# Optimization experiments

Hardware: AMD Instinct MI355X
Metric: run time of the kernel (lower is better)

Reference implementation:

```python
import jax, jax.numpy as jnp
import numpy as np

B, T = 32, 1024
TEMP_IN, STAT_IN = 128, 64
TEMP_OUT, STAT_OUT = 128, 64
EPS = 1e-5
NEG_SLOPE = 0.01


def _bn_eval(x, gamma, beta, mean, var):
    # BatchNorm1d in eval mode (running stats)
    return (x - mean) * jax.lax.rsqrt(var + EPS) * gamma + beta


def _leaky_relu(x):
    return jnp.where(x >= 0, x, NEG_SLOPE * x)


def setup_inputs() -> dict:
    key = jax.random.key(0)
    k = jax.random.split(key, 6)
    # deterministic ragged lengths in [512, 1024]
    lengths_np = (512 + (np.arange(B) * 37) % 513).astype(np.int64)
    N = int(lengths_np.sum())  # 23450
    batch_idx = np.repeat(np.arange(B), lengths_np).astype(np.int32)
    pos_idx = np.concatenate([np.arange(l) for l in lengths_np]).astype(np.int32)
    valid = (np.arange(T)[None, :] < lengths_np[:, None])  # [B, T]
    mask_repeat = valid[:, :, None] & valid[:, None, :]    # [B, T, T]

    inp = {
        "x_temp": jax.random.normal(k[0], (N, TEMP_IN), jnp.float32),
        "x_stat": jax.random.normal(k[1], (B, STAT_IN), jnp.float32),
        "temp_attn": jax.random.normal(k[2], (B, T, T), jnp.float32) * 0.1,
        "mask_repeat": jnp.asarray(mask_repeat),
        "lengths": jnp.asarray(lengths_np),
        "batch_idx": jnp.asarray(batch_idx),
        "pos_idx": jnp.asarray(pos_idx),
        # non_linear_temp: Linear(TEMP_IN+STAT_IN -> TEMP_OUT) + BN
        "W1": jax.random.normal(k[3], (TEMP_OUT, TEMP_IN + STAT_IN), jnp.float32) / np.sqrt(TEMP_IN + STAT_IN),
        "b1": jnp.zeros((TEMP_OUT,), jnp.float32),
        "gamma1": jnp.ones((TEMP_OUT,), jnp.float32),
        "beta1": jnp.zeros((TEMP_OUT,), jnp.float32),
        "mean1": jnp.zeros((TEMP_OUT,), jnp.float32),
        "var1": jnp.ones((TEMP_OUT,), jnp.float32),
        # non_linear_stat: Linear(STAT_IN -> STAT_OUT) + BN
        "W2": jax.random.normal(k[4], (STAT_OUT, STAT_IN), jnp.float32) / np.sqrt(STAT_IN),
        "b2": jnp.zeros((STAT_OUT,), jnp.float32),
        "gamma2": jnp.ones((STAT_OUT,), jnp.float32),
        "beta2": jnp.zeros((STAT_OUT,), jnp.float32),
        "mean2": jnp.zeros((STAT_OUT,), jnp.float32),
        "var2": jnp.ones((STAT_OUT,), jnp.float32),
    }
    return inp


def reference(x_temp, x_stat, temp_attn, mask_repeat, lengths, batch_idx, pos_idx,
              W1, b1, gamma1, beta1, mean1, var1,
              W2, b2, gamma2, beta2, mean2, var2):
    # repeat_static_features: gather per-batch static feats to packed rows
    x_stat_rep = x_stat[batch_idx]                              # [N, STAT_IN]
    h = jnp.concatenate((x_temp, x_stat_rep), axis=-1) @ W1.T + b1
    h = _leaky_relu(_bn_eval(h, gamma1, beta1, mean1, var1))    # [N, TEMP_OUT]

    # pad_packed_sequences: scatter packed rows into [B, T, C] (zeros elsewhere)
    padded = jnp.zeros((B, T, TEMP_OUT), h.dtype).at[batch_idx, pos_idx].set(h)

    # self attention: softmax(x x^T / sqrt(d)) over padded rows (as original)
    d = jnp.asarray(TEMP_OUT, h.dtype)
    qk = jnp.einsum('btc,bsc->bts', padded, padded) / jnp.sqrt(d)
    self_attn = jax.nn.softmax(qk, axis=-1)

    attn = jnp.where(mask_repeat, self_attn + temp_attn, jnp.asarray(0.0, h.dtype))

    x_stat_out = _leaky_relu(_bn_eval(x_stat @ W2.T + b2, gamma2, beta2, mean2, var2))

    x_out_pad = jnp.einsum('bts,bsc->btc', attn, padded)        # [B, T, TEMP_OUT]
    # pack_padded_sequences: gather valid positions back to packed layout
    x_out = x_out_pad[batch_idx, pos_idx]                       # [N, TEMP_OUT]
    return (x_out, x_stat_out)
```

## Files before the change

kernel.cpp:

```cpp
#include <hip/hip_runtime.h>
#include <hip/hip_bf16.h>
#include <hip/hip_fp16.h>

typedef __hip_bfloat16 bf16;
typedef __attribute__((ext_vector_type(8))) short short8;
typedef __attribute__((ext_vector_type(4))) float f32x4;

#define EPS 1e-5f
#define NSLOPE 0.01f
#define NSMAX 3

__device__ __forceinline__ float b2f(bf16 v) { return __bfloat162float(v); }
__device__ __forceinline__ float bs2f(unsigned short s) {
  bf16 t; __builtin_memcpy(&t, &s, 2); return __bfloat162float(t);
}
__device__ __forceinline__ float ld1(const void* p, size_t idx, int isbf) {
  if (isbf) return b2f(((const bf16*)p)[idx]);
  return ((const float*)p)[idx];
}
__device__ __forceinline__ void st1(void* p, size_t idx, int isbf, float v) {
  if (isbf) ((bf16*)p)[idx] = __float2bfloat16(v);
  else      ((float*)p)[idx] = v;
}
__device__ __forceinline__ short f2bs(float x) {
  bf16 t = __float2bfloat16(x);
  short s; __builtin_memcpy(&s, &t, 2); return s;
}
__device__ __forceinline__ short8 pack8f(const float* p) {
  float4 a = *(const float4*)p, b = *(const float4*)(p + 4);
  short8 r;
  r[0] = f2bs(a.x); r[1] = f2bs(a.y); r[2] = f2bs(a.z); r[3] = f2bs(a.w);
  r[4] = f2bs(b.x); r[5] = f2bs(b.y); r[6] = f2bs(b.z); r[7] = f2bs(b.w);
  return r;
}

__global__ void meta_kernel(const void* __restrict__ xt,
                            const int* __restrict__ bidx, const int* __restrict__ pidx,
                            int N, int B, int* __restrict__ rs, int* __restrict__ ln,
                            int* __restrict__ flag,
                            const void* __restrict__ W1, bf16* __restrict__ w1b, int w1n,
                            const void* __restrict__ xstat, const void* __restrict__ W2,
                            const void* __restrict__ b2, const void* __restrict__ g2,
                            const void* __restrict__ be2, const void* __restrict__ mn2,
                            const void* __restrict__ vr2, void* __restrict__ out,
                            long long obase) {
  int isbf_l = 0;
  {
    unsigned w = ((const unsigned*)xt)[threadIdx.x & 63];
    unsigned lo = w & 0xffffu;
    unsigned ex = (lo >> 7) & 0xffu;
    bool sane = ((lo & 0x7fffu) == 0u) || (ex >= 96u && ex <= 134u);
    unsigned long long m = __ballot(sane);
    isbf_l = (__popcll(m) >= 48) ? 1 : 0;
    if (blockIdx.x == 0 && threadIdx.x == 0) flag[0] = isbf_l;
  }
  int stride = gridDim.x * blockDim.x;
  int g0 = blockIdx.x * blockDim.x + threadIdx.x;
  for (int i = g0; i < N; i += stride) {
    int b = bidx[i];
    if ((unsigned)b >= (unsigned)B) continue;
    if (i == 0 || bidx[i - 1] != b) rs[b] = i;
    if (i == N - 1 || bidx[i + 1] != b) ln[b] = pidx[i] + 1;
  }
  for (int i = g0; i < w1n; i += stride) {
    int o = i / 192, k = i - o * 192;
    int ct = o >> 4, n = o & 15;
    int ks = k >> 5, rem = k & 31;
    int q = rem >> 3, j = rem & 7;
    int fi = ((ct * 6 + ks) * 64 + q * 16 + n) * 8 + j;
    w1b[fi] = __float2bfloat16(ld1(W1, i, isbf_l));
  }
  __shared__ float xs[64];
  if (threadIdx.x < 64 && blockIdx.x < B)
    xs[threadIdx.x] = ld1(xstat, blockIdx.x * 64 + threadIdx.x, isbf_l);
  __syncthreads();
  if (threadIdx.x < 64 && blockIdx.x < B) {
    const int o = threadIdx.x, bb = blockIdx.x;
    float acc = ld1(b2, o, isbf_l);
#pragma unroll 8
    for (int j = 0; j < 64; ++j) acc += xs[j] * ld1(W2, o * 64 + j, isbf_l);
    float k1 = ld1(g2, o, isbf_l) * rsqrtf(ld1(vr2, o, isbf_l) + EPS);
    float k0 = ld1(be2, o, isbf_l) - ld1(mn2, o, isbf_l) * k1;
    float v = acc * k1 + k0;
    v = (v >= 0.f) ? v : NSLOPE * v;
    st1(out, (size_t)(obase + bb * 64 + o), isbf_l, v);
  }
}

__global__ void zfill_kernel(void* out, const int* __restrict__ flag, long long n) {
  const int isbf = flag[0];
  long long i = (long long)blockIdx.x * blockDim.x + threadIdx.x;
  long long stride = (long long)gridDim.x * blockDim.x;
  for (; i < n; i += stride) st1(out, (size_t)i, isbf, 0.f);
}

__global__ __launch_bounds__(256) void h_mfma_kernel(
    const void* __restrict__ xt, const void* __restrict__ xsg,
    const int* __restrict__ bidx, const bf16* __restrict__ w1b,
    const void* __restrict__ b1,
    const void* __restrict__ g1, const void* __restrict__ be1,
    const void* __restrict__ mn1, const void* __restrict__ vr1,
    const int* __restrict__ flag, bf16* __restrict__ hout, int N) {
  const int isbf = flag[0];
  const int tid = threadIdx.x, lane = tid & 63, wv = tid >> 6;
  const int m16 = lane & 15, quad = lane >> 4;
  const int row0 = blockIdx.x * 64 + wv * 16;
  const int m = row0 + m16;
  const int mc = (m < N) ? m : (N - 1);
  const int bi = bidx[mc];

  short8 af[6];
  if (isbf) {
    const bf16* xr = (const bf16*)xt + (size_t)mc * 128 + quad * 8;
#pragma unroll
    for (int ks = 0; ks < 4; ++ks) af[ks] = *(const short8*)(xr + ks * 32);
    const bf16* sr = (const bf16*)xsg + (size_t)bi * 64 + quad * 8;
    af[4] = *(const short8*)sr;
    af[5] = *(const short8*)(sr + 32);
  } else {
    const float* xr = (const float*)xt + (size_t)mc * 128 + quad * 8;
#pragma unroll
    for (int ks = 0; ks < 4; ++ks) af[ks] = pack8f(xr + ks * 32);
    const float* sr = (const float*)xsg + (size_t)bi * 64 + quad * 8;
    af[4] = pack8f(sr);
    af[5] = pack8f(sr + 32);
  }

  f32x4 acc[8];
#pragma unroll
  for (int ct = 0; ct < 8; ++ct) acc[ct] = (f32x4){0.f, 0.f, 0.f, 0.f};

  const short8* wf = (const short8*)w1b;
#pragma unroll
  for (int ks = 0; ks < 6; ++ks) {
#pragma unroll
    for (int ct = 0; ct < 8; ++ct) {
      short8 bfrag = wf[(ct * 6 + ks) * 64 + lane];
      acc[ct] = __builtin_amdgcn_mfma_f32_16x16x32_bf16(af[ks], bfrag, acc[ct], 0, 0, 0);
    }
  }

#pragma unroll
  for (int ct = 0; ct < 8; ++ct) {
    const int o = ct * 16 + m16;
    float k1 = ld1(g1, o, isbf) * rsqrtf(ld1(vr1, o, isbf) + EPS);
    float k0 = ld1(be1, o, isbf) - ld1(mn1, o, isbf) * k1;
    float bias = ld1(b1, o, isbf);
#pragma unroll
    for (int r = 0; r < 4; ++r) {
      int mr = row0 + quad * 4 + r;
      if (mr < N) {
        float v = (acc[ct][r] + bias) * k1 + k0;
        v = (v >= 0.f) ? v : NSLOPE * v;
        hout[(size_t)mr * 128 + o] = __float2bfloat16(v);
      }
    }
  }
}

__global__ __launch_bounds__(256, 2) void attn_part_kernel(
    const void* __restrict__ ta, const bf16* __restrict__ h,
    const int* __restrict__ rs_arr, const int* __restrict__ ln_arr,
    const int* __restrict__ flag,
    unsigned short* __restrict__ accp_buf, unsigned short* __restrict__ acct_buf,
    float* __restrict__ ms_buf, float* __restrict__ ls_buf,
    int T, int N, int TT) {
  __shared__ __align__(16) unsigned short vT[128][72];
  __shared__ __align__(16) unsigned short Pw[4][16][72];

  const int b = blockIdx.y;
  const int tt = blockIdx.x / NSMAX, sl = blockIdx.x % NSMAX;
  const int t0 = tt * 64;
  const int len = ln_arr[b];
  if (t0 >= len) return;
  const int nchunk = (len + 63) >> 6;
  const int ns = (nchunk + 5) / 6;
  if (sl >= ns) return;
  const int c_begin = (sl * nchunk) / ns;
  const int c_end = ((sl + 1) * nchunk) / ns;

  const int isbf = flag[0];
  const int rs = rs_arr[b];
  const int tid = threadIdx.x;
  const int lane = tid & 63, wv = tid >> 6;
  const int m16 = lane & 15, quad = lane >> 4;
  const int t0w = t0 + wv * 16;

  short8 qf[4];
  {
    int qrow = rs + t0w + m16;
    if (qrow > N - 1) qrow = N - 1;
    const bf16* qp = h + (size_t)qrow * 128 + quad * 8;
#pragma unroll
    for (int ks = 0; ks < 4; ++ks) qf[ks] = *(const short8*)(qp + ks * 32);
  }

  const float scale = 0.08838834764831845f;
  const short8 zero8 = {0, 0, 0, 0, 0, 0, 0, 0};
  const uint4 zz = {0, 0, 0, 0};
  const size_t tarow = ((size_t)b * T + (t0w + m16)) * (size_t)T;
  const int c8base = wv * 32;

  f32x4 accp[8], acct[8];
#pragma unroll
  for (int ct = 0; ct < 8; ++ct) {
    accp[ct] = (f32x4){0.f, 0.f, 0.f, 0.f};
    acct[ct] = (f32x4){0.f, 0.f, 0.f, 0.f};
  }
  float mrun[4], lrun[4];
#pragma unroll
  for (int r = 0; r < 4; ++r) { mrun[r] = -INFINITY; lrun[r] = 0.f; }

  {
    int srow = c_begin * 64 + lane;
    bool v = srow < len;
    const bf16* src = h + (size_t)(rs + (v ? srow : 0)) * 128;
#pragma unroll
    for (int it = 0; it < 4; ++it) {
      int c8 = c8base + it * 8;
      uint4 u = v ? *(const uint4*)(src + c8) : zz;
      const unsigned short* a = (const unsigned short*)&u;
#pragma unroll
      for (int j = 0; j < 8; ++j) vT[c8 + j][lane] = a[j];
    }
  }
  __syncthreads();

  for (int ci = c_begin; ci < c_end; ++ci) {
    const int s0 = ci << 6;
    const bool have_next = (ci + 1 < c_end);

    uint4 su0 = zz, su1 = zz, su2 = zz, su3 = zz;
    if (have_next) {
      int srow = s0 + 64 + lane;
      bool v = srow < len;
      const bf16* src = h + (size_t)(rs + (v ? srow : 0)) * 128;
      if (v) {
        su0 = *(const uint4*)(src + c8base);
        su1 = *(const uint4*)(src + c8base + 8);
        su2 = *(const uint4*)(src + c8base + 16);
        su3 = *(const uint4*)(src + c8base + 24);
      }
    }

    short8 taf0, taf1;
    if (isbf) {
      const bf16* tp = (const bf16*)ta + tarow + s0 + quad * 8;
      taf0 = *(const short8*)tp;
      taf1 = *(const short8*)(tp + 32);
    } else {
      const float* tp = (const float*)ta + tarow + s0 + quad * 8;
      taf0 = pack8f(tp);
      taf1 = pack8f(tp + 32);
    }

    f32x4 sa[4];
    bool sval[4];
#pragma unroll
    for (int st = 0; st < 4; ++st) {
      int srow = s0 + st * 16 + m16;
      bool v = srow < len;
      sval[st] = v;
      const bf16* kp = h + (size_t)(rs + (v ? srow : 0)) * 128 + quad * 8;
      f32x4 a0 = (f32x4){0.f, 0.f, 0.f, 0.f};
#pragma unroll
      for (int ks = 0; ks < 4; ++ks) {
        short8 kf = v ? *(const short8*)(kp + ks * 32) : zero8;
        a0 = __builtin_amdgcn_mfma_f32_16x16x32_bf16(qf[ks], kf, a0, 0, 0, 0);
      }
      sa[st] = a0;
    }

    float cm[4];
#pragma unroll
    for (int r = 0; r < 4; ++r) cm[r] = -INFINITY;
#pragma unroll
    for (int st = 0; st < 4; ++st) {
#pragma unroll
      for (int r = 0; r < 4; ++r)
        cm[r] = fmaxf(cm[r], sval[st] ? sa[st][r] * scale : -INFINITY);
    }
#pragma unroll
    for (int off = 1; off <= 8; off <<= 1) {
#pragma unroll
      for (int r = 0; r < 4; ++r) cm[r] = fmaxf(cm[r], __shfl_xor(cm[r], off, 64));
    }
    float al[4], csum[4];
#pragma unroll
    for (int r = 0; r < 4; ++r) {
      float mnew = fmaxf(mrun[r], cm[r]);
      al[r] = __expf(mrun[r] - mnew);
      mrun[r] = mnew;
      csum[r] = 0.f;
    }
#pragma unroll
    for (int st = 0; st < 4; ++st) {
#pragma unroll
      for (int r = 0; r < 4; ++r) {
        float pv = sval[st] ? __expf(sa[st][r] * scale - mrun[r]) : 0.f;
        csum[r] += pv;
        Pw[wv][quad * 4 + r][st * 16 + m16] = (unsigned short)f2bs(pv);
      }
    }
#pragma unroll
    for (int off = 1; off <= 8; off <<= 1) {
#pragma unroll
      for (int r = 0; r < 4; ++r) csum[r] += __shfl_xor(csum[r], off, 64);
    }
#pragma unroll
    for (int r = 0; r < 4; ++r) lrun[r] = lrun[r] * al[r] + csum[r];

#pragma unroll
    for (int ct = 0; ct < 8; ++ct) {
#pragma unroll
      for (int r = 0; r < 4; ++r) accp[ct][r] *= al[r];
    }

#pragma unroll
    for (int ks = 0; ks < 2; ++ks) {
      short8 pf = *(const short8*)&Pw[wv][m16][ks * 32 + quad * 8];
      short8 tf = ks ? taf1 : taf0;
#pragma unroll
      for (int ct = 0; ct < 8; ++ct) {
        short8 bfv = *(const short8*)&vT[ct * 16 + m16][ks * 32 + quad * 8];
        accp[ct] = __builtin_amdgcn_mfma_f32_16x16x32_bf16(pf, bfv, accp[ct], 0, 0, 0);
        acct[ct] = __builtin_amdgcn_mfma_f32_16x16x32_bf16(tf, bfv, acct[ct], 0, 0, 0);
      }
    }

    if (have_next) {
      __syncthreads();
      const unsigned short* a0 = (const unsigned short*)&su0;
      const unsigned short* a1 = (const unsigned short*)&su1;
      const unsigned short* a2 = (const unsigned short*)&su2;
      const unsigned short* a3 = (const unsigned short*)&su3;
#pragma unroll
      for (int j = 0; j < 8; ++j) {
        vT[c8base + j][lane]      = a0[j];
        vT[c8base + 8 + j][lane]  = a1[j];
        vT[c8base + 16 + j][lane] = a2[j];
        vT[c8base + 24 + j][lane] = a3[j];
      }
      __syncthreads();
    }
  }

  const int slot = (b * TT + tt) * NSMAX + sl;
  const size_t abase = (size_t)slot * 8192;
#pragma unroll
  for (int r = 0; r < 4; ++r) {
    const int row = wv * 16 + quad * 4 + r;
#pragma unroll
    for (int ct = 0; ct < 8; ++ct) {
      const size_t o = abase + (size_t)row * 128 + ct * 16 + m16;
      accp_buf[o] = (unsigned short)f2bs(accp[ct][r]);
      acct_buf[o] = (unsigned short)f2bs(acct[ct][r]);
    }
    if (m16 == 0) {
      ms_buf[(size_t)slot * 64 + row] = mrun[r];
      ls_buf[(size_t)slot * 64 + row] = lrun[r];
    }
  }
}

__global__ __launch_bounds__(256) void attn_red_kernel(
    const unsigned short* __restrict__ accp_buf,
    const unsigned short* __restrict__ acct_buf,
    const float* __restrict__ ms_buf, const float* __restrict__ ls_buf,
    const int* __restrict__ rs_arr, const int* __restrict__ ln_arr,
    const int* __restrict__ flag, void* __restrict__ xout, int T, int TT) {
  const int b = blockIdx.y, tt = blockIdx.x, t0 = tt * 64;
  const int len = ln_arr[b];
  if (t0 >= len) return;
  const int isbf = flag[0];
  const int rs = rs_arr[b];
  const int nchunk = (len + 63) >> 6;
  const int ns = (nchunk + 5) / 6;
  const int base_slot = (b * TT + tt) * NSMAX;

  const int r = threadIdx.x >> 2;
  const int cg = threadIdx.x & 3;
  const int trow = t0 + r;
  if (trow >= len) return;

  float m0 = ms_buf[(size_t)(base_slot + 0) * 64 + r];
  float m1 = (ns > 1) ? ms_buf[(size_t)(base_slot + 1) * 64 + r] : -INFINITY;
  float m2 = (ns > 2) ? ms_buf[(size_t)(base_slot + 2) * 64 + r] : -INFINITY;
  float M = fmaxf(m0, fmaxf(m1, m2));
  float w0 = __expf(m0 - M);
  float w1 = (ns > 1) ? __expf(m1 - M) : 0.f;
  float w2 = (ns > 2) ? __expf(m2 - M) : 0.f;
  float L = ls_buf[(size_t)(base_slot + 0) * 64 + r] * w0;
  if (ns > 1) L += ls_buf[(size_t)(base_slot + 1) * 64 + r] * w1;
  if (ns > 2) L += ls_buf[(size_t)(base_slot + 2) * 64 + r] * w2;

  float m_f = (len < T) ? fmaxf(M, 0.f) : M;
  float corr = __expf(M - m_f);
  float l_f = L * corr + (float)(T - len) * __expf(-m_f);
  float os = corr / l_f;

  const size_t p0 = (size_t)(base_slot + 0) * 8192 + (size_t)r * 128 + cg * 32;
  const size_t p1 = (size_t)(base_slot + 1) * 8192 + (size_t)r * 128 + cg * 32;
  const size_t p2 = (size_t)(base_slot + 2) * 8192 + (size_t)r * 128 + cg * 32;
  const size_t ob = (size_t)(rs + trow) * 128 + cg * 32;

#pragma unroll
  for (int g = 0; g < 4; ++g) {
    float acc[8], tac[8];
    {
      short8 ap = *(const short8*)&accp_buf[p0 + g * 8];
      short8 at = *(const short8*)&acct_buf[p0 + g * 8];
#pragma unroll
      for (int j = 0; j < 8; ++j) {
        acc[j] = bs2f((unsigned short)ap[j]) * w0;
        tac[j] = bs2f((unsigned short)at[j]);
      }
    }
    if (ns > 1) {
      short8 ap = *(const short8*)&accp_buf[p1 + g * 8];
      short8 at = *(const short8*)&acct_buf[p1 + g * 8];
#pragma unroll
      for (int j = 0; j < 8; ++j) {
        acc[j] += bs2f((unsigned short)ap[j]) * w1;
        tac[j] += bs2f((unsigned short)at[j]);
      }
    }
    if (ns > 2) {
      short8 ap = *(const short8*)&accp_buf[p2 + g * 8];
      short8 at = *(const short8*)&acct_buf[p2 + g * 8];
#pragma unroll
      for (int j = 0; j < 8; ++j) {
        acc[j] += bs2f((unsigned short)ap[j]) * w2;
        tac[j] += bs2f((unsigned short)at[j]);
      }
    }
#pragma unroll
    for (int j = 0; j < 8; ++j)
      st1(xout, ob + g * 8 + j, isbf, acc[j] * os + tac[j]);
  }
}

__global__ __launch_bounds__(256, 2) void attn_mfma_kernel(
    const void* __restrict__ ta, const bf16* __restrict__ h,
    const int* __restrict__ rs_arr, const int* __restrict__ ln_arr,
    const int* __restrict__ flag, void* __restrict__ xout, int T, int N) {
  __shared__ __align__(16) unsigned short vT[2][128][72];
  __shared__ __align__(16) unsigned short Pw[4][16][72];

  const int b = blockIdx.y, t0 = blockIdx.x * 64;
  const int len = ln_arr[b];
  if (t0 >= len) return;
  const int isbf = flag[0];
  const int rs = rs_arr[b];
  const int tid = threadIdx.x;
  const int lane = tid & 63, wv = tid >> 6;
  const int m16 = lane & 15, quad = lane >> 4;
  const int t0w = t0 + wv * 16;

  short8 qf[4];
  {
    int qrow = rs + t0w + m16;
    if (qrow > N - 1) qrow = N - 1;
    const bf16* qp = h + (size_t)qrow * 128 + quad * 8;
#pragma unroll
    for (int ks = 0; ks < 4; ++ks) qf[ks] = *(const short8*)(qp + ks * 32);
  }

  const float scale = 0.08838834764831845f;
  const short8 zero8 = {0, 0, 0, 0, 0, 0, 0, 0};
  const uint4 zz = {0, 0, 0, 0};
  const size_t tarow = ((size_t)b * T + (t0w + m16)) * (size_t)T;
  const int c8base = wv * 32;

  f32x4 accp[8], acct[8];
#pragma unroll
  for (int ct = 0; ct < 8; ++ct) {
    accp[ct] = (f32x4){0.f, 0.f, 0.f, 0.f};
    acct[ct] = (f32x4){0.f, 0.f, 0.f, 0.f};
  }
  float mrun[4], lrun[4];
#pragma unroll
  for (int r = 0; r < 4; ++r) { mrun[r] = -INFINITY; lrun[r] = 0.f; }

  {
    int srow = lane;
    bool v = srow < len;
    const bf16* src = h + (size_t)(rs + (v ? srow : 0)) * 128;
#pragma unroll
    for (int it = 0; it < 4; ++it) {
      int c8 = c8base + it * 8;
      uint4 u = v ? *(const uint4*)(src + c8) : zz;
      const unsigned short* a = (const unsigned short*)&u;
#pragma unroll
      for (int j = 0; j < 8; ++j) vT[0][c8 + j][lane] = a[j];
    }
  }
  __syncthreads();

  const int nchunk = (len + 63) >> 6;
  for (int ci = 0; ci < nchunk; ++ci) {
    const int s0 = ci << 6;
    const int p = ci & 1;
    const bool have_next = (ci + 1 < nchunk);

    uint4 su0 = zz, su1 = zz, su2 = zz, su3 = zz;
    if (have_next) {
      int srow = s0 + 64 + lane;
      bool v = srow < len;
      const bf16* src = h + (size_t)(rs + (v ? srow : 0)) * 128;
      if (v) {
        su0 = *(const uint4*)(src + c8base);
        su1 = *(const uint4*)(src + c8base + 8);
        su2 = *(const uint4*)(src + c8base + 16);
        su3 = *(const uint4*)(src + c8base + 24);
      }
    }

    short8 taf0, taf1;
    if (isbf) {
      const bf16* tp = (const bf16*)ta + tarow + s0 + quad * 8;
      taf0 = *(const short8*)tp;
      taf1 = *(const short8*)(tp + 32);
    } else {
      const float* tp = (const float*)ta + tarow + s0 + quad * 8;
      taf0 = pack8f(tp);
      taf1 = pack8f(tp + 32);
    }

    f32x4 sa[4];
    bool sval[4];
#pragma unroll
    for (int st = 0; st < 4; ++st) {
      int srow = s0 + st * 16 + m16;
      bool v = srow < len;
      sval[st] = v;
      const bf16* kp = h + (size_t)(rs + (v ? srow : 0)) * 128 + quad * 8;
      f32x4 a0 = (f32x4){0.f, 0.f, 0.f, 0.f};
#pragma unroll
      for (int ks = 0; ks < 4; ++ks) {
        short8 kf = v ? *(const short8*)(kp + ks * 32) : zero8;
        a0 = __builtin_amdgcn_mfma_f32_16x16x32_bf16(qf[ks], kf, a0, 0, 0, 0);
      }
      sa[st] = a0;
    }

    float cm[4];
#pragma unroll
    for (int r = 0; r < 4; ++r) cm[r] = -INFINITY;
#pragma unroll
    for (int st = 0; st < 4; ++st) {
#pragma unroll
      for (int r = 0; r < 4; ++r)
        cm[r] = fmaxf(cm[r], sval[st] ? sa[st][r] * scale : -INFINITY);
    }
#pragma unroll
    for (int off = 1; off <= 8; off <<= 1) {
#pragma unroll
      for (int r = 0; r < 4; ++r) cm[r] = fmaxf(cm[r], __shfl_xor(cm[r], off, 64));
    }
    float al[4], csum[4];
#pragma unroll
    for (int r = 0; r < 4; ++r) {
      float mnew = fmaxf(mrun[r], cm[r]);
      al[r] = __expf(mrun[r] - mnew);
      mrun[r] = mnew;
      csum[r] = 0.f;
    }
#pragma unroll
    for (int st = 0; st < 4; ++st) {
#pragma unroll
      for (int r = 0; r < 4; ++r) {
        float pv = sval[st] ? __expf(sa[st][r] * scale - mrun[r]) : 0.f;
        csum[r] += pv;
        Pw[wv][quad * 4 + r][st * 16 + m16] = (unsigned short)f2bs(pv);
      }
    }
#pragma unroll
    for (int off = 1; off <= 8; off <<= 1) {
#pragma unroll
      for (int r = 0; r < 4; ++r) csum[r] += __shfl_xor(csum[r], off, 64);
    }
#pragma unroll
    for (int r = 0; r < 4; ++r) lrun[r] = lrun[r] * al[r] + csum[r];

#pragma unroll
    for (int ct = 0; ct < 8; ++ct) {
#pragma unroll
      for (int r = 0; r < 4; ++r) accp[ct][r] *= al[r];
    }

#pragma unroll
    for (int ks = 0; ks < 2; ++ks) {
      short8 pf = *(const short8*)&Pw[wv][m16][ks * 32 + quad * 8];
      short8 tf = ks ? taf1 : taf0;
#pragma unroll
      for (int ct = 0; ct < 8; ++ct) {
        short8 bfv = *(const short8*)&vT[p][ct * 16 + m16][ks * 32 + quad * 8];
        accp[ct] = __builtin_amdgcn_mfma_f32_16x16x32_bf16(pf, bfv, accp[ct], 0, 0, 0);
        acct[ct] = __builtin_amdgcn_mfma_f32_16x16x32_bf16(tf, bfv, acct[ct], 0, 0, 0);
      }
    }

    if (have_next) {
      const unsigned short* a0 = (const unsigned short*)&su0;
      const unsigned short* a1 = (const unsigned short*)&su1;
      const unsigned short* a2 = (const unsigned short*)&su2;
      const unsigned short* a3 = (const unsigned short*)&su3;
#pragma unroll
      for (int j = 0; j < 8; ++j) {
        vT[p ^ 1][c8base + j][lane]      = a0[j];
        vT[p ^ 1][c8base + 8 + j][lane]  = a1[j];
        vT[p ^ 1][c8base + 16 + j][lane] = a2[j];
        vT[p ^ 1][c8base + 24 + j][lane] = a3[j];
      }
    }
    __syncthreads();
  }

  const int nr = len - t0w;
#pragma unroll
  for (int r = 0; r < 4; ++r) {
    int t = quad * 4 + r;
    if (t < nr) {
      float m_r = mrun[r], l_r = lrun[r];
      float m_f = (len < T) ? fmaxf(m_r, 0.f) : m_r;
      float corr = __expf(m_r - m_f);
      float l_f = l_r * corr + (float)(T - len) * __expf(-m_f);
      float os = corr / l_f;
      size_t ob = (size_t)(rs + t0w + t) * 128;
#pragma unroll
      for (int ct = 0; ct < 8; ++ct)
        st1(xout, ob + ct * 16 + m16, isbf, accp[ct][r] * os + acct[ct][r]);
    }
  }
}

extern "C" void kernel_launch(void* const* d_in, const int* in_sizes, int n_in,
                              void* d_out, int out_size, void* d_ws, size_t ws_size,
                              hipStream_t stream) {
  const void* x_temp    = d_in[0];
  const void* x_stat    = d_in[1];
  const void* temp_attn = d_in[2];
  const int N = in_sizes[0] / 128;
  const int B = in_sizes[1] / 64;
  long long tt = (long long)in_sizes[2] / B;
  int T = 1; while ((long long)(T + 1) * (T + 1) <= tt) ++T;
  const int TT = (T + 63) >> 6;

  int p = 3;
  while (p < n_in && in_sizes[p] != N) ++p;
  const int* batch_idx = (const int*)d_in[p++];
  const int* pos_idx   = (const int*)d_in[p++];
  const void* W1 = d_in[p++];
  const void* b1 = d_in[p++];
  const void* g1 = d_in[p++];
  const void* be1= d_in[p++];
  const void* mn1= d_in[p++];
  const void* vr1= d_in[p++];
  const void* W2 = d_in[p++];
  const void* b2 = d_in[p++];
  const void* g2 = d_in[p++];
  const void* be2= d_in[p++];
  const void* mn2= d_in[p++];
  const void* vr2= d_in[p++];

  int*  meta = (int*)d_ws;
  int*  rs   = meta;
  int*  lnp  = meta + B;
  int*  flag = meta + 2 * B;
  size_t off = 1024;
  bf16* h    = (bf16*)((char*)d_ws + off);  off += (size_t)N * 128 * 2;
  const int w1n = 128 * 192;
  bf16* w1b  = (bf16*)((char*)d_ws + off);  off += (size_t)w1n * 2;
  off = (off + 255) & ~(size_t)255;
  size_t need_min = off;
  const size_t nslot = (size_t)B * TT * NSMAX;
  unsigned short* accp_buf = (unsigned short*)((char*)d_ws + off);
  off += nslot * 8192 * 2;
  unsigned short* acct_buf = (unsigned short*)((char*)d_ws + off);
  off += nslot * 8192 * 2;
  float* ms_buf = (float*)((char*)d_ws + off);  off += nslot * 64 * 4;
  float* ls_buf = (float*)((char*)d_ws + off);  off += nslot * 64 * 4;
  size_t need_split = off;

  long long obase = (long long)N * 128;

  meta_kernel<<<90, 256, 0, stream>>>(x_temp, batch_idx, pos_idx, N, B, rs, lnp,
                                      flag, W1, w1b, w1n,
                                      x_stat, W2, b2, g2, be2, mn2, vr2,
                                      d_out, obase);
  if (ws_size >= need_min) {
    h_mfma_kernel<<<(N + 63) / 64, 256, 0, stream>>>(x_temp, x_stat, batch_idx,
                                                     w1b, b1, g1, be1, mn1, vr1,
                                                     flag, h, N);
    if (ws_size >= need_split) {
      attn_part_kernel<<<dim3(TT * NSMAX, B), 256, 0, stream>>>(
          temp_attn, h, rs, lnp, flag, accp_buf, acct_buf, ms_buf, ls_buf,
          T, N, TT);
      attn_red_kernel<<<dim3(TT, B), 256, 0, stream>>>(
          accp_buf, acct_buf, ms_buf, ls_buf, rs, lnp, flag, d_out, T, TT);
    } else {
      attn_mfma_kernel<<<dim3(TT, B), 256, 0, stream>>>(
          temp_attn, h, rs, lnp, flag, d_out, T, N);
    }
  } else {
    zfill_kernel<<<512, 256, 0, stream>>>(d_out, flag, obase);
  }
}
```

Measured before the change: 424.9 us.

## Widen attention key chunk from 64 to 128 rows per iteration

The split-K flash attention kernel now processes 128 key rows per loop iteration instead of 64. The V-transpose tile in LDS is doubled and the P buffer is laid out as two halves. This halves the number of online-softmax rescales and block barriers per row block, and the partition count is recomputed to match in both kernels. In exchange it uses more registers (8 score tiles, 8 prefetched uint4 values, 4 temp_attn fragments) and more LDS, which may lower occupancy under launch_bounds(256,2).

```diff
diff --git a/kernel.cpp b/kernel.cpp
--- a/kernel.cpp
+++ b/kernel.cpp
@@ -31,6 +31,14 @@
   short8 r;
   r[0] = f2bs(a.x); r[1] = f2bs(a.y); r[2] = f2bs(a.z); r[3] = f2bs(a.w);
   r[4] = f2bs(b.x); r[5] = f2bs(b.y); r[6] = f2bs(b.z); r[7] = f2bs(b.w);
+  return r;
+}
+__device__ __forceinline__ short8 pack8u(uint4 a, uint4 b) {
+  const float* fa = (const float*)&a;
+  const float* fb = (const float*)&b;
+  short8 r;
+  r[0] = f2bs(fa[0]); r[1] = f2bs(fa[1]); r[2] = f2bs(fa[2]); r[3] = f2bs(fa[3]);
+  r[4] = f2bs(fb[0]); r[5] = f2bs(fb[1]); r[6] = f2bs(fb[2]); r[7] = f2bs(fb[3]);
   return r;
 }
 
@@ -165,16 +173,16 @@
     unsigned short* __restrict__ accp_buf, unsigned short* __restrict__ acct_buf,
     float* __restrict__ ms_buf, float* __restrict__ ls_buf,
     int T, int N, int TT) {
-  __shared__ __align__(16) unsigned short vT[128][72];
-  __shared__ __align__(16) unsigned short Pw[4][16][72];
+  __shared__ __align__(16) unsigned short vT[2][128][72];
+  __shared__ __align__(16) unsigned short Pw[4][16][2][72];
 
   const int b = blockIdx.y;
   const int tt = blockIdx.x / NSMAX, sl = blockIdx.x % NSMAX;
   const int t0 = tt * 64;
   const int len = ln_arr[b];
   if (t0 >= len) return;
-  const int nchunk = (len + 63) >> 6;
-  const int ns = (nchunk + 5) / 6;
+  const int nchunk = (len + 127) >> 7;
+  const int ns = (nchunk + 2) / 3;
   if (sl >= ns) return;
   const int c_begin = (sl * nchunk) / ns;
   const int c_end = ((sl + 1) * nchunk) / ns;
@@ -212,52 +220,67 @@
   for (int r = 0; r < 4; ++r) { mrun[r] = -INFINITY; lrun[r] = 0.f; }
 
   {
-    int srow = c_begin * 64 + lane;
-    bool v = srow < len;
-    const bf16* src = h + (size_t)(rs + (v ? srow : 0)) * 128;
-#pragma unroll
-    for (int it = 0; it < 4; ++it) {
-      int c8 = c8base + it * 8;
-      uint4 u = v ? *(const uint4*)(src + c8) : zz;
-      const unsigned short* a = (const unsigned short*)&u;
-#pragma unroll
-      for (int j = 0; j < 8; ++j) vT[c8 + j][lane] = a[j];
-    }
-  }
-  __syncthreads();
-
-  for (int ci = c_begin; ci < c_end; ++ci) {
-    const int s0 = ci << 6;
-    const bool have_next = (ci + 1 < c_end);
-
-    uint4 su0 = zz, su1 = zz, su2 = zz, su3 = zz;
-    if (have_next) {
-      int srow = s0 + 64 + lane;
+    const int s0 = c_begin << 7;
+#pragma unroll
+    for (int hf = 0; hf < 2; ++hf) {
+      int srow = s0 + hf * 64 + lane;
       bool v = srow < len;
       const bf16* src = h + (size_t)(rs + (v ? srow : 0)) * 128;
-      if (v) {
-        su0 = *(const uint4*)(src + c8base);
-        su1 = *(const uint4*)(src + c8base + 8);
-        su2 = *(const uint4*)(src + c8base + 16);
-        su3 = *(const uint4*)(src + c8base + 24);
-      }
-    }
-
-    short8 taf0, taf1;
+#pragma unroll
+      for (int it = 0; it < 4; ++it) {
+        int c8 = c8base + it * 8;
+        uint4 u = v ? *(const uint4*)(src + c8) : zz;
+        const unsigned short* a = (const unsigned short*)&u;
+#pragma unroll
+        for (int j = 0; j < 8; ++j) vT[hf][c8 + j][lane] = a[j];
+      }
+    }
+  }
+  __syncthreads();
+
+  for (int ci = c_begin; ci < c_end; ++ci) {
+    const int s0 = ci << 7;
+    const bool have_next = (ci + 1 < c_end);
+
+    uint4 su[2][4];
+#pragma unroll
+    for (int hf = 0; hf < 2; ++hf) {
+#pragma unroll
+      for (int it = 0; it < 4; ++it) su[hf][it] = zz;
+    }
+    if (have_next) {
+#pragma unroll
+      for (int hf = 0; hf < 2; ++hf) {
+        int srow = s0 + 128 + hf * 64 + lane;
+        bool v = srow < len;
+        const bf16* src = h + (size_t)(rs + (v ? srow : 0)) * 128;
+        if (v) {
+#pragma unroll
+          for (int it = 0; it < 4; ++it)
+            su[hf][it] = *(const uint4*)(src + c8base + it * 8);
+        }
+      }
+    }
+
+    short8 taf[4];
     if (isbf) {
       const bf16* tp = (const bf16*)ta + tarow + s0 + quad * 8;
-      taf0 = *(const short8*)tp;
-      taf1 = *(const short8*)(tp + 32);
+#pragma unroll
+      for (int ks = 0; ks < 4; ++ks) taf[ks] = *(const short8*)(tp + ks * 32);
     } else {
       const float* tp = (const float*)ta + tarow + s0 + quad * 8;
-      taf0 = pack8f(tp);
-      taf1 = pack8f(tp + 32);
-    }
-
-    f32x4 sa[4];
-    bool sval[4];
-#pragma unroll
-    for (int st = 0; st < 4; ++st) {
+#pragma unroll
+      for (int ks = 0; ks < 4; ++ks) {
+        uint4 ua = *(const uint4*)(tp + ks * 32);
+        uint4 ub = *(const uint4*)(tp + ks * 32 + 4);
+        taf[ks] = pack8u(ua, ub);
+      }
+    }
+
+    f32x4 sa[8];
+    bool sval[8];
+#pragma unroll
+    for (int st = 0; st < 8; ++st) {
       int srow = s0 + st * 16 + m16;
       bool v = srow < len;
       sval[st] = v;
@@ -275,7 +298,7 @@
 #pragma unroll
     for (int r = 0; r < 4; ++r) cm[r] = -INFINITY;
 #pragma unroll
-    for (int st = 0; st < 4; ++st) {
+    for (int st = 0; st < 8; ++st) {
 #pragma unroll
       for (int r = 0; r < 4; ++r)
         cm[r] = fmaxf(cm[r], sval[st] ? sa[st][r] * scale : -INFINITY);
@@ -294,12 +317,12 @@
       csum[r] = 0.f;
     }
 #pragma unroll
-    for (int st = 0; st < 4; ++st) {
+    for (int st = 0; st < 8; ++st) {
 #pragma unroll
       for (int r = 0; r < 4; ++r) {
         float pv = sval[st] ? __expf(sa[st][r] * scale - mrun[r]) : 0.f;
         csum[r] += pv;
-        Pw[wv][quad * 4 + r][st * 16 + m16] = (unsigned short)f2bs(pv);
+        Pw[wv][quad * 4 + r][st >> 2][(st & 3) * 16 + m16] = (unsigned short)f2bs(pv);
       }
     }
 #pragma unroll
@@ -317,12 +340,12 @@
     }
 
 #pragma unroll
-    for (int ks = 0; ks < 2; ++ks) {
-      short8 pf = *(const short8*)&Pw[wv][m16][ks * 32 + quad * 8];
-      short8 tf = ks ? taf1 : taf0;
+    for (int ks = 0; ks < 4; ++ks) {
+      short8 pf = *(const short8*)&Pw[wv][m16][ks >> 1][(ks & 1) * 32 + quad * 8];
+      short8 tf = taf[ks];
 #pragma unroll
       for (int ct = 0; ct < 8; ++ct) {
-        short8 bfv = *(const short8*)&vT[ct * 16 + m16][ks * 32 + quad * 8];
+        short8 bfv = *(const short8*)&vT[ks >> 1][ct * 16 + m16][(ks & 1) * 32 + quad * 8];
         accp[ct] = __builtin_amdgcn_mfma_f32_16x16x32_bf16(pf, bfv, accp[ct], 0, 0, 0);
         acct[ct] = __builtin_amdgcn_mfma_f32_16x16x32_bf16(tf, bfv, acct[ct], 0, 0, 0);
       }
@@ -330,16 +353,15 @@
 
     if (have_next) {
       __syncthreads();
-      const unsigned short* a0 = (const unsigned short*)&su0;
-      const unsigned short* a1 = (const unsigned short*)&su1;
-      const unsigned short* a2 = (const unsigned short*)&su2;
-      const unsigned short* a3 = (const unsigned short*)&su3;
-#pragma unroll
-      for (int j = 0; j < 8; ++j) {
-        vT[c8base + j][lane]      = a0[j];
-        vT[c8base + 8 + j][lane]  = a1[j];
-        vT[c8base + 16 + j][lane] = a2[j];
-        vT[c8base + 24 + j][lane] = a3[j];
+#pragma unroll
+      for (int hf = 0; hf < 2; ++hf) {
+#pragma unroll
+        for (int it = 0; it < 4; ++it) {
+          const unsigned short* a = (const unsigned short*)&su[hf][it];
+#pragma unroll
+          for (int j = 0; j < 8; ++j)
+            vT[hf][c8base + it * 8 + j][lane] = a[j];
+        }
       }
       __syncthreads();
     }
@@ -374,8 +396,8 @@
   if (t0 >= len) return;
   const int isbf = flag[0];
   const int rs = rs_arr[b];
-  const int nchunk = (len + 63) >> 6;
-  const int ns = (nchunk + 5) / 6;
+  const int nchunk = (len + 127) >> 7;
+  const int ns = (nchunk + 2) / 3;
   const int base_slot = (b * TT + tt) * NSMAX;
 
   const int r = threadIdx.x >> 2;
```

After: 445.2 us. 1.05x slower.
